# Kernel optimization log

Hardware: AMD Instinct MI355X
Metric: run time of the kernel (lower is better)

Reference implementation:

```python
import jax, jax.numpy as jnp
import numpy as np

N_NODES = 50000
N_EDGES = 800000
D = 128  # node_dim == edge_dim == out_dim


def setup_inputs() -> dict:
    key = jax.random.key(0)
    ks = jax.random.split(key, 8)
    x = jax.random.normal(ks[0], (N_NODES, D), dtype=jnp.float32)
    edge_feat = jax.random.normal(ks[1], (N_EDGES, D), dtype=jnp.float32)
    src = jax.random.randint(ks[2], (N_EDGES,), 0, N_NODES)
    dst = jax.random.randint(ks[3], (N_EDGES,), 0, N_NODES)
    # xavier-ish init scales
    W_fc = jax.random.normal(ks[4], (D, D), dtype=jnp.float32) * (1.0 / np.sqrt(D))
    W_rel = jax.random.normal(ks[5], (D, 2 * D), dtype=jnp.float32) * (1.0 / np.sqrt(2 * D))
    b_rel = jnp.zeros((D,), dtype=jnp.float32)
    W_attn = jax.random.normal(ks[6], (1, 2 * D), dtype=jnp.float32) * (1.0 / np.sqrt(2 * D))
    return {"x": x, "edge_feat": edge_feat, "src": src, "dst": dst,
            "W_fc": W_fc, "W_rel": W_rel, "b_rel": b_rel, "W_attn": W_attn}


def reference(x, edge_feat, src, dst, W_fc, W_rel, b_rel, W_attn):
    n = x.shape[0]
    # z = fc(input), no bias
    z = x @ W_fc.T                                    # [N, D]
    z_src = z[src]                                    # [E, D] gather
    z_dst = z[dst]                                    # [E, D] gather
    # end = relation_fc(cat([edge_h, z_dst]))
    end = jnp.concatenate([edge_feat, z_dst], axis=1) @ W_rel.T + b_rel  # [E, D]
    # a = attn_fc(cat([z_src, end])); e = leaky_relu(a)
    a = (jnp.concatenate([z_src, end], axis=1) @ W_attn.T)[:, 0]         # [E]
    e = jax.nn.leaky_relu(a, negative_slope=0.01)
    # segment softmax over each destination node's mailbox
    m = jax.ops.segment_max(e, dst, num_segments=n)   # [N]
    ex = jnp.exp(e - m[dst])                          # [E]
    denom = jax.ops.segment_sum(ex, dst, num_segments=n)                 # [N]
    alpha = ex / denom[dst]                           # [E]
    # weighted scatter-sum of src z into dst
    h = jax.ops.segment_sum(alpha[:, None] * z_src, dst, num_segments=n)  # [N, D]
    return h
```

## Files before the change

kernel.cpp:

```cpp
#include <hip/hip_runtime.h>

#define D 128

__global__ __launch_bounds__(256) void precompute_g(
    const float* __restrict__ Wrel,
    const float* __restrict__ brel,
    const float* __restrict__ Wattn,
    float* __restrict__ gbuf)
{
    int k = threadIdx.x;
    float acc = 0.f;
    for (int j = 0; j < 128; ++j)
        acc += Wattn[128 + j] * Wrel[j * 256 + k];
    gbuf[k] = acc;
    if (k == 0) {
        float c = 0.f;
        for (int j = 0; j < 128; ++j) c += Wattn[128 + j] * brel[j];
        gbuf[256] = c;
    }
}

__global__ __launch_bounds__(256) void zgemm(
    const float* __restrict__ x, const float* __restrict__ W,
    float* __restrict__ z, int nrows)
{
    __shared__ float xs[64][132];
    __shared__ float ws[128][132];
    int tid = threadIdx.x;
    int row0 = blockIdx.x * 64;

    for (int i = tid; i < 128 * 32; i += 256) {
        int c = i >> 5, k4 = (i & 31) << 2;
        float4 v = *(const float4*)&W[c * 128 + k4];
        *(float4*)&ws[c][k4] = v;
    }
    for (int i = tid; i < 64 * 32; i += 256) {
        int r = i >> 5, k4 = (i & 31) << 2;
        int gr = row0 + r;
        float4 v = make_float4(0.f, 0.f, 0.f, 0.f);
        if (gr < nrows) v = *(const float4*)&x[(size_t)gr * D + k4];
        *(float4*)&xs[r][k4] = v;
    }
    __syncthreads();

    int tx = tid & 15, ty = tid >> 4;
    float acc[4][8] = {};
    for (int k = 0; k < 128; ++k) {
        float xv[4], wv[8];
#pragma unroll
        for (int i = 0; i < 4; ++i) xv[i] = xs[ty * 4 + i][k];
#pragma unroll
        for (int j = 0; j < 8; ++j) wv[j] = ws[tx + 16 * j][k];
#pragma unroll
        for (int i = 0; i < 4; ++i)
#pragma unroll
            for (int j = 0; j < 8; ++j) acc[i][j] += xv[i] * wv[j];
    }
#pragma unroll
    for (int i = 0; i < 4; ++i) {
        int gr = row0 + ty * 4 + i;
        if (gr >= nrows) continue;
#pragma unroll
        for (int j = 0; j < 8; ++j)
            z[(size_t)gr * D + tx + 16 * j] = acc[i][j];
    }
}

__global__ __launch_bounds__(256) void node_pq(
    const float* __restrict__ z, const float* __restrict__ attn,
    const float* __restrict__ gbuf, float* __restrict__ pbuf,
    float* __restrict__ qbuf, int N)
{
    int lane = threadIdx.x & 63;
    int node = blockIdx.x * 4 + (threadIdx.x >> 6);
    if (node >= N) return;
    float2 v = *(const float2*)&z[(size_t)node * D + lane * 2];
    float2 a = *(const float2*)&attn[lane * 2];
    float2 g = *(const float2*)&gbuf[128 + lane * 2];
    float ps = v.x * a.x + v.y * a.y;
    float qs = v.x * g.x + v.y * g.y;
#pragma unroll
    for (int off = 32; off >= 1; off >>= 1) {
        ps += __shfl_xor(ps, off);
        qs += __shfl_xor(qs, off);
    }
    if (lane == 0) { pbuf[node] = ps; qbuf[node] = qs; }
}

__global__ __launch_bounds__(256) void edge_logits(
    const float* __restrict__ ef,
    const int* __restrict__ src, const int* __restrict__ dst,
    const float* __restrict__ gbuf,
    const float* __restrict__ pbuf, const float* __restrict__ qbuf,
    float* __restrict__ ebuf, int* __restrict__ cnt, int E)
{
    int tid = threadIdx.x;
    int lane = tid & 15;
    int e = blockIdx.x * 16 + (tid >> 4);
    if (e >= E) return;
    const float* efr = ef + (size_t)e * D;
    float acc = 0.f;
#pragma unroll
    for (int p = 0; p < 2; ++p) {
        int idx = lane * 4 + p * 64;
        float4 a4  = *(const float4*)&efr[idx];
        float4 g14 = *(const float4*)&gbuf[idx];
        acc += a4.x * g14.x + a4.y * g14.y + a4.z * g14.z + a4.w * g14.w;
    }
#pragma unroll
    for (int off = 8; off >= 1; off >>= 1) acc += __shfl_xor(acc, off);
    if (lane == 0) {
        int d = dst[e];
        float a = acc + pbuf[src[e]] + qbuf[d] + gbuf[256];
        float ev = a > 0.f ? a : 0.01f * a;
        ebuf[e] = __expf(ev);
        atomicAdd(&cnt[d], 1);
    }
}

__global__ __launch_bounds__(256) void partial_sums(
    const int* __restrict__ cnt, int* __restrict__ bsum, int N)
{
    __shared__ int ws_[4];
    int tid = threadIdx.x, lane = tid & 63, wid = tid >> 6;
    int i0 = blockIdx.x * 1024 + tid * 4;
    int s = 0;
#pragma unroll
    for (int j = 0; j < 4; ++j) s += (i0 + j < N) ? cnt[i0 + j] : 0;
#pragma unroll
    for (int off = 32; off >= 1; off >>= 1) s += __shfl_xor(s, off);
    if (lane == 0) ws_[wid] = s;
    __syncthreads();
    if (tid == 0) bsum[blockIdx.x] = ws_[0] + ws_[1] + ws_[2] + ws_[3];
}

__global__ __launch_bounds__(256) void scan_partials(
    const int* __restrict__ bsum, int* __restrict__ boffs, int nb)
{
    __shared__ int ws_[4];
    int tid = threadIdx.x, lane = tid & 63, wid = tid >> 6;
    int v = (tid < nb) ? bsum[tid] : 0;
    int incl = v;
#pragma unroll
    for (int off = 1; off < 64; off <<= 1) {
        int t = __shfl_up(incl, off);
        if (lane >= off) incl += t;
    }
    if (lane == 63) ws_[wid] = incl;
    __syncthreads();
    int woff = 0;
    for (int w = 0; w < wid; ++w) woff += ws_[w];
    if (tid < nb) boffs[tid] = woff + incl - v;
}

__global__ __launch_bounds__(256) void local_scan(
    const int* __restrict__ cnt, const int* __restrict__ boffs,
    int* __restrict__ offs, int N, int E)
{
    __shared__ int ws_[4];
    int tid = threadIdx.x, lane = tid & 63, wid = tid >> 6;
    int i0 = blockIdx.x * 1024 + tid * 4;
    int v[4];
    int tsum = 0;
#pragma unroll
    for (int j = 0; j < 4; ++j) {
        v[j] = (i0 + j < N) ? cnt[i0 + j] : 0;
        tsum += v[j];
    }
    int incl = tsum;
#pragma unroll
    for (int off = 1; off < 64; off <<= 1) {
        int t = __shfl_up(incl, off);
        if (lane >= off) incl += t;
    }
    if (lane == 63) ws_[wid] = incl;
    __syncthreads();
    int woff = 0;
    for (int w = 0; w < wid; ++w) woff += ws_[w];
    int run = boffs[blockIdx.x] + woff + incl - tsum;
#pragma unroll
    for (int j = 0; j < 4; ++j) {
        if (i0 + j < N) offs[i0 + j] = run;
        run += v[j];
    }
    if (blockIdx.x == 0 && tid == 0) offs[N] = E;
}

__global__ __launch_bounds__(256) void scatter_csr(
    const int* __restrict__ src, const int* __restrict__ dst,
    const float* __restrict__ ebuf, const int* __restrict__ offs,
    int* __restrict__ cursor, int2* __restrict__ spack, int E)
{
    int e = blockIdx.x * 256 + threadIdx.x;
    if (e >= E) return;
    int d = dst[e];
    int pos = atomicAdd(&cursor[d], 1);
    spack[offs[d] + pos] = make_int2(src[e], __float_as_int(ebuf[e]));
}

__global__ __launch_bounds__(256) void node_gather(
    const float* __restrict__ z, const int2* __restrict__ spack,
    const int* __restrict__ offs, float* __restrict__ out, int N)
{
    int tid = threadIdx.x, lane = tid & 63;
    int node = blockIdx.x * 4 + (tid >> 6);
    if (node >= N) return;
    int o0 = offs[node], o1 = offs[node + 1];
    float2 acc = make_float2(0.f, 0.f);
    float denom = 0.f;
    int j = o0;
    for (; j + 1 < o1; j += 2) {
        int2 p0 = spack[j], p1 = spack[j + 1];
        float x0 = __int_as_float(p0.y), x1 = __int_as_float(p1.y);
        float2 v0 = *(const float2*)&z[(size_t)p0.x * D + lane * 2];
        float2 v1 = *(const float2*)&z[(size_t)p1.x * D + lane * 2];
        denom += x0 + x1;
        acc.x += x0 * v0.x + x1 * v1.x;
        acc.y += x0 * v0.y + x1 * v1.y;
    }
    if (j < o1) {
        int2 p0 = spack[j];
        float x0 = __int_as_float(p0.y);
        float2 v0 = *(const float2*)&z[(size_t)p0.x * D + lane * 2];
        denom += x0;
        acc.x += x0 * v0.x;
        acc.y += x0 * v0.y;
    }
    if (o1 > o0) {
        float inv = 1.f / denom;
        acc.x *= inv;
        acc.y *= inv;
    }
    *(float2*)&out[(size_t)node * D + lane * 2] = acc;
}

extern "C" void kernel_launch(void* const* d_in, const int* in_sizes, int n_in,
                              void* d_out, int out_size, void* d_ws, size_t ws_size,
                              hipStream_t stream) {
    const float* x     = (const float*)d_in[0];
    const float* ef    = (const float*)d_in[1];
    const int*   src   = (const int*)d_in[2];
    const int*   dst   = (const int*)d_in[3];
    const float* Wfc   = (const float*)d_in[4];
    const float* Wrel  = (const float*)d_in[5];
    const float* brel  = (const float*)d_in[6];
    const float* Wattn = (const float*)d_in[7];
    int N = in_sizes[0] / D;
    int E = in_sizes[2];
    int nb = (N + 1023) / 1024;
    float* out = (float*)d_out;

    float* z      = (float*)d_ws;
    int2*  spack  = (int2*)(z + (size_t)N * D);
    float* ebuf   = (float*)(spack + E);
    float* pbuf   = ebuf + E;
    float* qbuf   = pbuf + N;
    int*   cnt    = (int*)(qbuf + N);
    int*   cursor = cnt + N;
    int*   offs   = cursor + N;
    int*   bsum   = offs + N + 1;
    int*   boffs  = bsum + 256;
    float* gbuf   = (float*)(boffs + 256);

    hipMemsetAsync(cnt, 0, 2 * (size_t)N * sizeof(int), stream);

    precompute_g<<<1, 256, 0, stream>>>(Wrel, brel, Wattn, gbuf);
    zgemm<<<(N + 63) / 64, 256, 0, stream>>>(x, Wfc, z, N);
    node_pq<<<(N + 3) / 4, 256, 0, stream>>>(z, Wattn, gbuf, pbuf, qbuf, N);
    edge_logits<<<(E + 15) / 16, 256, 0, stream>>>(ef, src, dst, gbuf, pbuf, qbuf,
                                                   ebuf, cnt, E);
    partial_sums<<<nb, 256, 0, stream>>>(cnt, bsum, N);
    scan_partials<<<1, 256, 0, stream>>>(bsum, boffs, nb);
    local_scan<<<nb, 256, 0, stream>>>(cnt, boffs, offs, N, E);
    scatter_csr<<<(E + 255) / 256, 256, 0, stream>>>(src, dst, ebuf, offs, cursor,
                                                     spack, E);
    node_gather<<<(N + 3) / 4, 256, 0, stream>>>(z, spack, offs, out, N);
}
```

Before: 301.9 us.

## Fuse node projections into GEMM, count degrees early, and scatter logits directly

Degree counting moves into the weight-precompute kernel so the CSR scan can finish before edge logits are computed. That lets the logit kernel write exp-logits straight into CSR slots and drops the intermediate ebuf and the separate scatter pass. The per-node p/q projections are fused into the z GEMM epilogue, and W is read from global/L1 instead of being staged in shared memory. The gather loop is unrolled to 4 edges. Costs: an extra pass over dst for counting, and uncached-style global W reads in the GEMM inner loop.

```diff
diff --git a/kernel.cpp b/kernel.cpp
--- a/kernel.cpp
+++ b/kernel.cpp
@@ -2,38 +2,41 @@
 
 #define D 128
 
-__global__ __launch_bounds__(256) void precompute_g(
+__global__ __launch_bounds__(256) void g_and_count(
     const float* __restrict__ Wrel,
     const float* __restrict__ brel,
     const float* __restrict__ Wattn,
-    float* __restrict__ gbuf)
-{
-    int k = threadIdx.x;
-    float acc = 0.f;
-    for (int j = 0; j < 128; ++j)
-        acc += Wattn[128 + j] * Wrel[j * 256 + k];
-    gbuf[k] = acc;
-    if (k == 0) {
-        float c = 0.f;
-        for (int j = 0; j < 128; ++j) c += Wattn[128 + j] * brel[j];
-        gbuf[256] = c;
-    }
-}
-
-__global__ __launch_bounds__(256) void zgemm(
+    const int* __restrict__ dst,
+    float* __restrict__ gbuf,
+    int* __restrict__ cnt, int E)
+{
+    if (blockIdx.x == 0) {
+        int k = threadIdx.x;
+        float acc = 0.f;
+        for (int j = 0; j < 128; ++j)
+            acc += Wattn[128 + j] * Wrel[j * 256 + k];
+        gbuf[k] = acc;
+        if (k == 0) {
+            float c = 0.f;
+            for (int j = 0; j < 128; ++j) c += Wattn[128 + j] * brel[j];
+            gbuf[256] = c;
+        }
+    } else {
+        int e = (blockIdx.x - 1) * 256 + threadIdx.x;
+        if (e < E) atomicAdd(&cnt[dst[e]], 1);
+    }
+}
+
+__global__ __launch_bounds__(256) void zgemm_pq(
     const float* __restrict__ x, const float* __restrict__ W,
-    float* __restrict__ z, int nrows)
+    const float* __restrict__ attn, const float* __restrict__ gbuf,
+    float* __restrict__ z, float* __restrict__ pbuf, float* __restrict__ qbuf,
+    int nrows)
 {
     __shared__ float xs[64][132];
-    __shared__ float ws[128][132];
     int tid = threadIdx.x;
     int row0 = blockIdx.x * 64;
 
-    for (int i = tid; i < 128 * 32; i += 256) {
-        int c = i >> 5, k4 = (i & 31) << 2;
-        float4 v = *(const float4*)&W[c * 128 + k4];
-        *(float4*)&ws[c][k4] = v;
-    }
     for (int i = tid; i < 64 * 32; i += 256) {
         int r = i >> 5, k4 = (i & 31) << 2;
         int gr = row0 + r;
@@ -45,54 +48,122 @@
 
     int tx = tid & 15, ty = tid >> 4;
     float acc[4][8] = {};
-    for (int k = 0; k < 128; ++k) {
-        float xv[4], wv[8];
-#pragma unroll
-        for (int i = 0; i < 4; ++i) xv[i] = xs[ty * 4 + i][k];
-#pragma unroll
-        for (int j = 0; j < 8; ++j) wv[j] = ws[tx + 16 * j][k];
+    for (int k = 0; k < 128; k += 4) {
+        float4 xv[4], wv[8];
+#pragma unroll
+        for (int j = 0; j < 8; ++j)
+            wv[j] = *(const float4*)&W[(size_t)(tx + 16 * j) * D + k];
 #pragma unroll
         for (int i = 0; i < 4; ++i)
-#pragma unroll
-            for (int j = 0; j < 8; ++j) acc[i][j] += xv[i] * wv[j];
+            xv[i] = *(const float4*)&xs[ty * 4 + i][k];
+#pragma unroll
+        for (int i = 0; i < 4; ++i)
+#pragma unroll
+            for (int j = 0; j < 8; ++j)
+                acc[i][j] += xv[i].x * wv[j].x + xv[i].y * wv[j].y +
+                             xv[i].z * wv[j].z + xv[i].w * wv[j].w;
+    }
+
+    float a1[8], g2[8];
+#pragma unroll
+    for (int j = 0; j < 8; ++j) {
+        a1[j] = attn[tx + 16 * j];
+        g2[j] = gbuf[128 + tx + 16 * j];
     }
 #pragma unroll
     for (int i = 0; i < 4; ++i) {
         int gr = row0 + ty * 4 + i;
         if (gr >= nrows) continue;
-#pragma unroll
-        for (int j = 0; j < 8; ++j)
+        float ps = 0.f, qs = 0.f;
+#pragma unroll
+        for (int j = 0; j < 8; ++j) {
             z[(size_t)gr * D + tx + 16 * j] = acc[i][j];
-    }
-}
-
-__global__ __launch_bounds__(256) void node_pq(
-    const float* __restrict__ z, const float* __restrict__ attn,
-    const float* __restrict__ gbuf, float* __restrict__ pbuf,
-    float* __restrict__ qbuf, int N)
-{
-    int lane = threadIdx.x & 63;
-    int node = blockIdx.x * 4 + (threadIdx.x >> 6);
-    if (node >= N) return;
-    float2 v = *(const float2*)&z[(size_t)node * D + lane * 2];
-    float2 a = *(const float2*)&attn[lane * 2];
-    float2 g = *(const float2*)&gbuf[128 + lane * 2];
-    float ps = v.x * a.x + v.y * a.y;
-    float qs = v.x * g.x + v.y * g.y;
-#pragma unroll
-    for (int off = 32; off >= 1; off >>= 1) {
-        ps += __shfl_xor(ps, off);
-        qs += __shfl_xor(qs, off);
-    }
-    if (lane == 0) { pbuf[node] = ps; qbuf[node] = qs; }
-}
-
-__global__ __launch_bounds__(256) void edge_logits(
+            ps += a1[j] * acc[i][j];
+            qs += g2[j] * acc[i][j];
+        }
+#pragma unroll
+        for (int off = 8; off >= 1; off >>= 1) {
+            ps += __shfl_xor(ps, off);
+            qs += __shfl_xor(qs, off);
+        }
+        if (tx == 0) { pbuf[gr] = ps; qbuf[gr] = qs; }
+    }
+}
+
+__global__ __launch_bounds__(256) void partial_sums(
+    const int* __restrict__ cnt, int* __restrict__ bsum, int N)
+{
+    __shared__ int ws_[4];
+    int tid = threadIdx.x, lane = tid & 63, wid = tid >> 6;
+    int i0 = blockIdx.x * 1024 + tid * 4;
+    int s = 0;
+#pragma unroll
+    for (int j = 0; j < 4; ++j) s += (i0 + j < N) ? cnt[i0 + j] : 0;
+#pragma unroll
+    for (int off = 32; off >= 1; off >>= 1) s += __shfl_xor(s, off);
+    if (lane == 0) ws_[wid] = s;
+    __syncthreads();
+    if (tid == 0) bsum[blockIdx.x] = ws_[0] + ws_[1] + ws_[2] + ws_[3];
+}
+
+__global__ __launch_bounds__(256) void scan_partials(
+    const int* __restrict__ bsum, int* __restrict__ boffs, int nb)
+{
+    __shared__ int ws_[4];
+    int tid = threadIdx.x, lane = tid & 63, wid = tid >> 6;
+    int v = (tid < nb) ? bsum[tid] : 0;
+    int incl = v;
+#pragma unroll
+    for (int off = 1; off < 64; off <<= 1) {
+        int t = __shfl_up(incl, off);
+        if (lane >= off) incl += t;
+    }
+    if (lane == 63) ws_[wid] = incl;
+    __syncthreads();
+    int woff = 0;
+    for (int w = 0; w < wid; ++w) woff += ws_[w];
+    if (tid < nb) boffs[tid] = woff + incl - v;
+}
+
+__global__ __launch_bounds__(256) void local_scan(
+    const int* __restrict__ cnt, const int* __restrict__ boffs,
+    int* __restrict__ offs, int* __restrict__ cursor, int N, int E)
+{
+    __shared__ int ws_[4];
+    int tid = threadIdx.x, lane = tid & 63, wid = tid >> 6;
+    int i0 = blockIdx.x * 1024 + tid * 4;
+    int v[4];
+    int tsum = 0;
+#pragma unroll
+    for (int j = 0; j < 4; ++j) {
+        v[j] = (i0 + j < N) ? cnt[i0 + j] : 0;
+        tsum += v[j];
+    }
+    int incl = tsum;
+#pragma unroll
+    for (int off = 1; off < 64; off <<= 1) {
+        int t = __shfl_up(incl, off);
+        if (lane >= off) incl += t;
+    }
+    if (lane == 63) ws_[wid] = incl;
+    __syncthreads();
+    int woff = 0;
+    for (int w = 0; w < wid; ++w) woff += ws_[w];
+    int run = boffs[blockIdx.x] + woff + incl - tsum;
+#pragma unroll
+    for (int j = 0; j < 4; ++j) {
+        if (i0 + j < N) { offs[i0 + j] = run; cursor[i0 + j] = run; }
+        run += v[j];
+    }
+    if (blockIdx.x == 0 && tid == 0) offs[N] = E;
+}
+
+__global__ __launch_bounds__(256) void edge_logits_scatter(
     const float* __restrict__ ef,
     const int* __restrict__ src, const int* __restrict__ dst,
     const float* __restrict__ gbuf,
     const float* __restrict__ pbuf, const float* __restrict__ qbuf,
-    float* __restrict__ ebuf, int* __restrict__ cnt, int E)
+    int* __restrict__ cursor, int2* __restrict__ spack, int E)
 {
     int tid = threadIdx.x;
     int lane = tid & 15;
@@ -110,92 +181,12 @@
 #pragma unroll
     for (int off = 8; off >= 1; off >>= 1) acc += __shfl_xor(acc, off);
     if (lane == 0) {
-        int d = dst[e];
-        float a = acc + pbuf[src[e]] + qbuf[d] + gbuf[256];
+        int s = src[e], d = dst[e];
+        float a = acc + pbuf[s] + qbuf[d] + gbuf[256];
         float ev = a > 0.f ? a : 0.01f * a;
-        ebuf[e] = __expf(ev);
-        atomicAdd(&cnt[d], 1);
-    }
-}
-
-__global__ __launch_bounds__(256) void partial_sums(
-    const int* __restrict__ cnt, int* __restrict__ bsum, int N)
-{
-    __shared__ int ws_[4];
-    int tid = threadIdx.x, lane = tid & 63, wid = tid >> 6;
-    int i0 = blockIdx.x * 1024 + tid * 4;
-    int s = 0;
-#pragma unroll
-    for (int j = 0; j < 4; ++j) s += (i0 + j < N) ? cnt[i0 + j] : 0;
-#pragma unroll
-    for (int off = 32; off >= 1; off >>= 1) s += __shfl_xor(s, off);
-    if (lane == 0) ws_[wid] = s;
-    __syncthreads();
-    if (tid == 0) bsum[blockIdx.x] = ws_[0] + ws_[1] + ws_[2] + ws_[3];
-}
-
-__global__ __launch_bounds__(256) void scan_partials(
-    const int* __restrict__ bsum, int* __restrict__ boffs, int nb)
-{
-    __shared__ int ws_[4];
-    int tid = threadIdx.x, lane = tid & 63, wid = tid >> 6;
-    int v = (tid < nb) ? bsum[tid] : 0;
-    int incl = v;
-#pragma unroll
-    for (int off = 1; off < 64; off <<= 1) {
-        int t = __shfl_up(incl, off);
-        if (lane >= off) incl += t;
-    }
-    if (lane == 63) ws_[wid] = incl;
-    __syncthreads();
-    int woff = 0;
-    for (int w = 0; w < wid; ++w) woff += ws_[w];
-    if (tid < nb) boffs[tid] = woff + incl - v;
-}
-
-__global__ __launch_bounds__(256) void local_scan(
-    const int* __restrict__ cnt, const int* __restrict__ boffs,
-    int* __restrict__ offs, int N, int E)
-{
-    __shared__ int ws_[4];
-    int tid = threadIdx.x, lane = tid & 63, wid = tid >> 6;
-    int i0 = blockIdx.x * 1024 + tid * 4;
-    int v[4];
-    int tsum = 0;
-#pragma unroll
-    for (int j = 0; j < 4; ++j) {
-        v[j] = (i0 + j < N) ? cnt[i0 + j] : 0;
-        tsum += v[j];
-    }
-    int incl = tsum;
-#pragma unroll
-    for (int off = 1; off < 64; off <<= 1) {
-        int t = __shfl_up(incl, off);
-        if (lane >= off) incl += t;
-    }
-    if (lane == 63) ws_[wid] = incl;
-    __syncthreads();
-    int woff = 0;
-    for (int w = 0; w < wid; ++w) woff += ws_[w];
-    int run = boffs[blockIdx.x] + woff + incl - tsum;
-#pragma unroll
-    for (int j = 0; j < 4; ++j) {
-        if (i0 + j < N) offs[i0 + j] = run;
-        run += v[j];
-    }
-    if (blockIdx.x == 0 && tid == 0) offs[N] = E;
-}
-
-__global__ __launch_bounds__(256) void scatter_csr(
-    const int* __restrict__ src, const int* __restrict__ dst,
-    const float* __restrict__ ebuf, const int* __restrict__ offs,
-    int* __restrict__ cursor, int2* __restrict__ spack, int E)
-{
-    int e = blockIdx.x * 256 + threadIdx.x;
-    if (e >= E) return;
-    int d = dst[e];
-    int pos = atomicAdd(&cursor[d], 1);
-    spack[offs[d] + pos] = make_int2(src[e], __float_as_int(ebuf[e]));
+        int pos = atomicAdd(&cursor[d], 1);
+        spack[pos] = make_int2(s, __float_as_int(__expf(ev)));
+    }
 }
 
 __global__ __launch_bounds__(256) void node_gather(
@@ -209,16 +200,19 @@
     float2 acc = make_float2(0.f, 0.f);
     float denom = 0.f;
     int j = o0;
-    for (; j + 1 < o1; j += 2) {
-        int2 p0 = spack[j], p1 = spack[j + 1];
-        float x0 = __int_as_float(p0.y), x1 = __int_as_float(p1.y);
+    for (; j + 3 < o1; j += 4) {
+        int2 p0 = spack[j], p1 = spack[j + 1], p2 = spack[j + 2], p3 = spack[j + 3];
         float2 v0 = *(const float2*)&z[(size_t)p0.x * D + lane * 2];
         float2 v1 = *(const float2*)&z[(size_t)p1.x * D + lane * 2];
-        denom += x0 + x1;
-        acc.x += x0 * v0.x + x1 * v1.x;
-        acc.y += x0 * v0.y + x1 * v1.y;
-    }
-    if (j < o1) {
+        float2 v2 = *(const float2*)&z[(size_t)p2.x * D + lane * 2];
+        float2 v3 = *(const float2*)&z[(size_t)p3.x * D + lane * 2];
+        float x0 = __int_as_float(p0.y), x1 = __int_as_float(p1.y);
+        float x2 = __int_as_float(p2.y), x3 = __int_as_float(p3.y);
+        denom += (x0 + x1) + (x2 + x3);
+        acc.x += x0 * v0.x + x1 * v1.x + x2 * v2.x + x3 * v3.x;
+        acc.y += x0 * v0.y + x1 * v1.y + x2 * v2.y + x3 * v3.y;
+    }
+    for (; j < o1; ++j) {
         int2 p0 = spack[j];
         float x0 = __int_as_float(p0.y);
         float2 v0 = *(const float2*)&z[(size_t)p0.x * D + lane * 2];
@@ -252,27 +246,26 @@
 
     float* z      = (float*)d_ws;
     int2*  spack  = (int2*)(z + (size_t)N * D);
-    float* ebuf   = (float*)(spack + E);
-    float* pbuf   = ebuf + E;
+    float* pbuf   = (float*)(spack + E);
     float* qbuf   = pbuf + N;
     int*   cnt    = (int*)(qbuf + N);
     int*   cursor = cnt + N;
     int*   offs   = cursor + N;
-    int*   bsum   = offs + N + 1;
+    int*   bsum   = offs + N + 16;
     int*   boffs  = bsum + 256;
     float* gbuf   = (float*)(boffs + 256);
 
-    hipMemsetAsync(cnt, 0, 2 * (size_t)N * sizeof(int), stream);
-
-    precompute_g<<<1, 256, 0, stream>>>(Wrel, brel, Wattn, gbuf);
-    zgemm<<<(N + 63) / 64, 256, 0, stream>>>(x, Wfc, z, N);
-    node_pq<<<(N + 3) / 4, 256, 0, stream>>>(z, Wattn, gbuf, pbuf, qbuf, N);
-    edge_logits<<<(E + 15) / 16, 256, 0, stream>>>(ef, src, dst, gbuf, pbuf, qbuf,
-                                                   ebuf, cnt, E);
+    hipMemsetAsync(cnt, 0, (size_t)N * sizeof(int), stream);
+
+    g_and_count<<<1 + (E + 255) / 256, 256, 0, stream>>>(Wrel, brel, Wattn, dst,
+                                                         gbuf, cnt, E);
+    zgemm_pq<<<(N + 63) / 64, 256, 0, stream>>>(x, Wfc, Wattn, gbuf, z, pbuf,
+                                                qbuf, N);
     partial_sums<<<nb, 256, 0, stream>>>(cnt, bsum, N);
     scan_partials<<<1, 256, 0, stream>>>(bsum, boffs, nb);
-    local_scan<<<nb, 256, 0, stream>>>(cnt, boffs, offs, N, E);
-    scatter_csr<<<(E + 255) / 256, 256, 0, stream>>>(src, dst, ebuf, offs, cursor,
-                                                     spack, E);
+    local_scan<<<nb, 256, 0, stream>>>(cnt, boffs, offs, cursor, N, E);
+    edge_logits_scatter<<<(E + 15) / 16, 256, 0, stream>>>(ef, src, dst, gbuf,
+                                                           pbuf, qbuf, cursor,
+                                                           spack, E);
     node_gather<<<(N + 3) / 4, 256, 0, stream>>>(z, spack, offs, out, N);
 }
```

Measured after the change: 326.9 us. 8.3% more time.
